# Optimization experiments

Measured on AMD Instinct MI355X. Metric: run time of the kernel, lower is better.

Reference implementation:

```python
import jax, jax.numpy as jnp
import numpy as np

N_NODES = 50000


def _gcn_conv(x, W, b, src, dst, n):
    # PyG GCNConv: linear, then D^{-1/2}(A+I)D^{-1/2} aggregation, then bias.
    x = x @ W  # [N, out]
    loops = jnp.arange(n, dtype=src.dtype)
    src_f = jnp.concatenate([src, loops])  # add self-loops
    dst_f = jnp.concatenate([dst, loops])
    deg = jax.ops.segment_sum(jnp.ones_like(dst_f, dtype=x.dtype), dst_f, num_segments=n)
    dinv = jnp.where(deg > 0, jax.lax.rsqrt(deg), 0.0)
    norm = dinv[src_f] * dinv[dst_f]            # [E+N]
    msg = x[src_f] * norm[:, None]              # gather + scale
    out = jax.ops.segment_sum(msg, dst_f, num_segments=n)  # scatter-add
    return out + b


def setup_inputs() -> dict:
    key = jax.random.key(0)
    k1, k2, k3, k4 = jax.random.split(key, 4)
    ninp = 128
    emb = jax.random.normal(k1, (N_NODES, ninp), dtype=jnp.float32)
    emb = emb.at[0].set(0.0)  # padding_idx=0
    W1 = jax.random.normal(k2, (ninp, 2 * ninp), dtype=jnp.float32) * (1.0 / np.sqrt(ninp))
    b1 = jnp.zeros((2 * ninp,), dtype=jnp.float32)
    W2 = jax.random.normal(k3, (2 * ninp, ninp), dtype=jnp.float32) * (1.0 / np.sqrt(2 * ninp))
    b2 = jnp.zeros((ninp,), dtype=jnp.float32)
    edge_index = jax.random.randint(k4, (2, 800000), 0, N_NODES, dtype=jnp.int64)
    return {"emb": emb, "W1": W1, "b1": b1, "W2": W2, "b2": b2, "edge_index": edge_index}


def reference(emb, W1, b1, W2, b2, edge_index) -> jnp.ndarray:
    src, dst = edge_index[0], edge_index[1]
    h = _gcn_conv(emb, W1, b1, src, dst, N_NODES)   # [N, 2*ninp]
    # dropout in eval mode -> identity
    out = _gcn_conv(h, W2, b2, src, dst, N_NODES)   # [N, ninp]
    return out
```

## Files before the change

### kernel.cpp

```cpp
#include <hip/hip_runtime.h>

#define N_NODES 50000
#define N_EDGES 800000
#define NB 196

typedef unsigned int uint;
typedef short bf16x8 __attribute__((ext_vector_type(8)));
typedef float f32x4 __attribute__((ext_vector_type(4)));

__device__ __forceinline__ ushort f2bf(float f) {
    union { float f; uint u; } v; v.f = f;
    uint r = (v.u + 0x7FFFu + ((v.u >> 16) & 1u)) >> 16;
    return (ushort)r;
}
__device__ __forceinline__ float bf_lo(uint u) { return __uint_as_float(u << 16); }
__device__ __forceinline__ float bf_hi(uint u) { return __uint_as_float(u & 0xFFFF0000u); }

__global__ void k_tobf16(const float* __restrict__ in, uint* __restrict__ out) {
    int t = blockIdx.x * 256 + threadIdx.x;
    const float4* i4 = (const float4*)in + (size_t)t * 2;
    float4 v0 = i4[0], v1 = i4[1];
    uint4 o;
    o.x = (uint)f2bf(v0.x) | ((uint)f2bf(v0.y) << 16);
    o.y = (uint)f2bf(v0.z) | ((uint)f2bf(v0.w) << 16);
    o.z = (uint)f2bf(v1.x) | ((uint)f2bf(v1.y) << 16);
    o.w = (uint)f2bf(v1.z) | ((uint)f2bf(v1.w) << 16);
    ((uint4*)out)[t] = o;
}

__global__ void k_w12(const float* __restrict__ W1, const float* __restrict__ W2,
                      const float* __restrict__ b1, ushort* __restrict__ W12t,
                      float* __restrict__ bvec) {
    int n = threadIdx.x;
    int k = blockIdx.x;
    float s = 0.f;
    if (k < 128) {
        for (int m = 0; m < 256; ++m) s = fmaf(W1[(size_t)k * 256 + m], W2[(size_t)m * 128 + n], s);
        W12t[(size_t)n * 128 + k] = f2bf(s);
    } else {
        for (int m = 0; m < 256; ++m) s = fmaf(b1[m], W2[(size_t)m * 128 + n], s);
        bvec[n] = s;
    }
}


__global__ void k_zero(int* counts) {
    int i = blockIdx.x * 256 + threadIdx.x;
    if (i < N_NODES) counts[i] = 0;
}

__global__ void k_histrank(const int* __restrict__ dst, int* __restrict__ counts,
                           ushort* __restrict__ rank) {
    int e = blockIdx.x * 256 + threadIdx.x;
    if (e < N_EDGES) rank[e] = (ushort)atomicAdd(&counts[dst[e]], 1);
}

__global__ void k_blocksum(const int* __restrict__ counts, int* __restrict__ bsum) {
    __shared__ int lds[256];
    int t = threadIdx.x;
    int i = blockIdx.x * 256 + t;
    int v = (i < N_NODES) ? counts[i] : 0;
    lds[t] = v;
    __syncthreads();
    for (int off = 128; off > 0; off >>= 1) {
        if (t < off) lds[t] += lds[t + off];
        __syncthreads();
    }
    if (t == 0) bsum[blockIdx.x] = lds[0];
}

__global__ void k_scanb(const int* __restrict__ bsum, int* __restrict__ boff) {
    __shared__ int lds[256];
    int t = threadIdx.x;
    int v = (t < NB) ? bsum[t] : 0;
    lds[t] = v;
    __syncthreads();
    for (int off = 1; off < 256; off <<= 1) {
        int o = (t >= off) ? lds[t - off] : 0;
        __syncthreads();
        lds[t] += o;
        __syncthreads();
    }
    if (t < NB) boff[t] = lds[t] - v;
}

__global__ void k_scatter_rp(const int* __restrict__ counts, const int* __restrict__ boff,
                             int* __restrict__ row_ptr, float* __restrict__ dinv) {
    __shared__ int lds[256];
    int t = threadIdx.x;
    int i = blockIdx.x * 256 + t;
    int v = (i < N_NODES) ? counts[i] : 0;
    lds[t] = v;
    __syncthreads();
    for (int off = 1; off < 256; off <<= 1) {
        int o = (t >= off) ? lds[t - off] : 0;
        __syncthreads();
        lds[t] += o;
        __syncthreads();
    }
    if (i < N_NODES) {
        row_ptr[i] = boff[blockIdx.x] + lds[t] - v;
        dinv[i] = rsqrtf((float)(v + 1));
    }
    if (i == 0) row_ptr[N_NODES] = N_EDGES;
}

__global__ void k_fillr(const int* __restrict__ src, const int* __restrict__ dst,
                        const ushort* __restrict__ rank, const int* __restrict__ row_ptr,
                        const float* __restrict__ dinv, uint* __restrict__ csr) {
    int e = blockIdx.x * 256 + threadIdx.x;
    if (e >= N_EDGES) return;
    int s = src[e];
    int pos = row_ptr[dst[e]] + (int)rank[e];
    csr[pos] = ((uint)s << 16) | (uint)f2bf(dinv[s]);
}

template<bool NVEC>
__global__ void k_gather128h(const uint* __restrict__ xh, const uint* __restrict__ csr,
                             const int* __restrict__ rp, const float* __restrict__ dinv,
                             uint* __restrict__ outp, float* __restrict__ nvec) {
    int node = blockIdx.x * 4 + (threadIdx.x >> 6);
    int lane = threadIdx.x & 63;
    int q = lane >> 4;
    int fl = lane & 15;
    int beg = rp[node], end = rp[node + 1];
    const uint4* xb = (const uint4*)xh;
    float a[8];
    #pragma unroll
    for (int i = 0; i < 8; ++i) a[i] = 0.f;
    float sc = 0.f;

    for (int j = beg + q; j < end; j += 16) {
        int j1 = j + 4, j2 = j + 8, j3 = j + 12;
        uint e0 = csr[j];
        uint e1 = (j1 < end) ? csr[j1] : (e0 & 0xFFFF0000u);
        uint e2 = (j2 < end) ? csr[j2] : (e0 & 0xFFFF0000u);
        uint e3 = (j3 < end) ? csr[j3] : (e0 & 0xFFFF0000u);
        int s0 = e0 >> 16, s1 = e1 >> 16, s2 = e2 >> 16, s3 = e3 >> 16;
        float c0 = bf_lo(e0), c1 = bf_lo(e1), c2 = bf_lo(e2), c3 = bf_lo(e3);
        uint4 u0 = xb[(size_t)s0 * 16 + fl];
        uint4 u1 = xb[(size_t)s1 * 16 + fl];
        uint4 u2 = xb[(size_t)s2 * 16 + fl];
        uint4 u3 = xb[(size_t)s3 * 16 + fl];
        sc += c0 + c1 + c2 + c3;
        a[0] = fmaf(c0, bf_lo(u0.x), a[0]); a[1] = fmaf(c0, bf_hi(u0.x), a[1]);
        a[2] = fmaf(c0, bf_lo(u0.y), a[2]); a[3] = fmaf(c0, bf_hi(u0.y), a[3]);
        a[4] = fmaf(c0, bf_lo(u0.z), a[4]); a[5] = fmaf(c0, bf_hi(u0.z), a[5]);
        a[6] = fmaf(c0, bf_lo(u0.w), a[6]); a[7] = fmaf(c0, bf_hi(u0.w), a[7]);
        a[0] = fmaf(c1, bf_lo(u1.x), a[0]); a[1] = fmaf(c1, bf_hi(u1.x), a[1]);
        a[2] = fmaf(c1, bf_lo(u1.y), a[2]); a[3] = fmaf(c1, bf_hi(u1.y), a[3]);
        a[4] = fmaf(c1, bf_lo(u1.z), a[4]); a[5] = fmaf(c1, bf_hi(u1.z), a[5]);
        a[6] = fmaf(c1, bf_lo(u1.w), a[6]); a[7] = fmaf(c1, bf_hi(u1.w), a[7]);
        a[0] = fmaf(c2, bf_lo(u2.x), a[0]); a[1] = fmaf(c2, bf_hi(u2.x), a[1]);
        a[2] = fmaf(c2, bf_lo(u2.y), a[2]); a[3] = fmaf(c2, bf_hi(u2.y), a[3]);
        a[4] = fmaf(c2, bf_lo(u2.z), a[4]); a[5] = fmaf(c2, bf_hi(u2.z), a[5]);
        a[6] = fmaf(c2, bf_lo(u2.w), a[6]); a[7] = fmaf(c2, bf_hi(u2.w), a[7]);
        a[0] = fmaf(c3, bf_lo(u3.x), a[0]); a[1] = fmaf(c3, bf_hi(u3.x), a[1]);
        a[2] = fmaf(c3, bf_lo(u3.y), a[2]); a[3] = fmaf(c3, bf_hi(u3.y), a[3]);
        a[4] = fmaf(c3, bf_lo(u3.z), a[4]); a[5] = fmaf(c3, bf_hi(u3.z), a[5]);
        a[6] = fmaf(c3, bf_lo(u3.w), a[6]); a[7] = fmaf(c3, bf_hi(u3.w), a[7]);
    }
    #pragma unroll
    for (int off = 16; off < 64; off <<= 1) {
        #pragma unroll
        for (int i = 0; i < 8; ++i) a[i] += __shfl_xor(a[i], off);
        if (NVEC) sc += __shfl_xor(sc, off);
    }
    if (q == 0) {
        float dd = dinv[node];
        float dd2 = dd * dd;
        uint4 u = xb[(size_t)node * 16 + fl];
        float s[8] = { bf_lo(u.x), bf_hi(u.x), bf_lo(u.y), bf_hi(u.y),
                       bf_lo(u.z), bf_hi(u.z), bf_lo(u.w), bf_hi(u.w) };
        uint4 p;
        float o0 = fmaf(dd, a[0], dd2 * s[0]), o1 = fmaf(dd, a[1], dd2 * s[1]);
        float o2 = fmaf(dd, a[2], dd2 * s[2]), o3 = fmaf(dd, a[3], dd2 * s[3]);
        float o4 = fmaf(dd, a[4], dd2 * s[4]), o5 = fmaf(dd, a[5], dd2 * s[5]);
        float o6 = fmaf(dd, a[6], dd2 * s[6]), o7 = fmaf(dd, a[7], dd2 * s[7]);
        p.x = (uint)f2bf(o0) | ((uint)f2bf(o1) << 16);
        p.y = (uint)f2bf(o2) | ((uint)f2bf(o3) << 16);
        p.z = (uint)f2bf(o4) | ((uint)f2bf(o5) << 16);
        p.w = (uint)f2bf(o6) | ((uint)f2bf(o7) << 16);
        ((uint4*)outp)[(size_t)node * 16 + fl] = p;
        if (NVEC && fl == 0) nvec[node] = fmaf(dd, sc, dd2);
    }
}

__global__ void __launch_bounds__(256)
k_gemm_out(const ushort* __restrict__ A, const ushort* __restrict__ Wt,
           const float* __restrict__ nvec, const float* __restrict__ bvec,
           const float* __restrict__ b2, float* __restrict__ out) {
    constexpr int K = 128, NC = 128, KC = 4, TPW = 2;
    const int lane = threadIdx.x & 63;
    const int wave = threadIdx.x >> 6;
    const int row0 = blockIdx.x * 16;
    const int r = row0 + (lane & 15);
    const int ksub = (lane >> 4) * 8;

    f32x4 acc[TPW];
    int col[TPW];
    #pragma unroll
    for (int t = 0; t < TPW; ++t) {
        acc[t] = (f32x4){0.f, 0.f, 0.f, 0.f};
        col[t] = (wave * TPW + t) * 16 + (lane & 15);
    }
    #pragma unroll
    for (int kc = 0; kc < KC; ++kc) {
        bf16x8 af = *(const bf16x8*)(A + (size_t)r * K + kc * 32 + ksub);
        #pragma unroll
        for (int t = 0; t < TPW; ++t) {
            bf16x8 bf = *(const bf16x8*)(Wt + (size_t)col[t] * K + kc * 32 + ksub);
            acc[t] = __builtin_amdgcn_mfma_f32_16x16x32_bf16(af, bf, acc[t], 0, 0, 0);
        }
    }
    const int rb = row0 + (lane >> 4) * 4;
    float nv[4];
    #pragma unroll
    for (int e = 0; e < 4; ++e) nv[e] = nvec[rb + e];
    #pragma unroll
    for (int t = 0; t < TPW; ++t) {
        float bv = bvec[col[t]];
        float bb = b2[col[t]];
        #pragma unroll
        for (int e = 0; e < 4; ++e) {
            out[(size_t)(rb + e) * NC + col[t]] = acc[t][e] + nv[e] * bv + bb;
        }
    }
}

extern "C" void kernel_launch(void* const* d_in, const int* in_sizes, int n_in,
                              void* d_out, int out_size, void* d_ws, size_t ws_size,
                              hipStream_t stream) {
    const float* emb = (const float*)d_in[0];
    const float* W1  = (const float*)d_in[1];
    const float* b1  = (const float*)d_in[2];
    const float* W2  = (const float*)d_in[3];
    const float* b2  = (const float*)d_in[4];
    const int*   ei  = (const int*)d_in[5];
    const int* src = ei;
    const int* dst = ei + N_EDGES;

    char* ws = (char*)d_ws;
    float*  dinv    = (float*) (ws);
    int*    counts  = (int*)   (ws + (256ull << 10));
    int*    row_ptr = (int*)   (ws + (512ull << 10));
    int*    bsum    = (int*)   (ws + (768ull << 10));
    int*    boff    = (int*)   (ws + (772ull << 10));
    ushort* rank    = (ushort*)(ws + (1ull << 20));
    uint*   csr     = (uint*)  (ws + (3ull << 20));
    ushort* W12t    = (ushort*)(ws + (6656ull << 10));
    float*  bvec    = (float*) (ws + (6720ull << 10));
    float*  nvec    = (float*) (ws + (6784ull << 10));
    uint*   emb_h   = (uint*)  (ws + (7ull  << 20));
    uint*   G       = (uint*)  (ws + (20ull << 20));
    uint*   G2      = (uint*)  (ws + (33ull << 20));
    float*  out     = (float*)d_out;

    k_tobf16<<<N_NODES * 128 / 8 / 256, 256, 0, stream>>>(emb, emb_h);
    k_w12<<<129, 128, 0, stream>>>(W1, W2, b1, W12t, bvec);

    k_zero<<<NB, 256, 0, stream>>>(counts);
    k_histrank<<<(N_EDGES + 255) / 256, 256, 0, stream>>>(dst, counts, rank);
    k_blocksum<<<NB, 256, 0, stream>>>(counts, bsum);
    k_scanb<<<1, 256, 0, stream>>>(bsum, boff);
    k_scatter_rp<<<NB, 256, 0, stream>>>(counts, boff, row_ptr, dinv);
    k_fillr<<<(N_EDGES + 255) / 256, 256, 0, stream>>>(src, dst, rank, row_ptr, dinv, csr);

    k_gather128h<false><<<12500, 256, 0, stream>>>(emb_h, csr, row_ptr, dinv, G, nullptr);
    k_gather128h<true><<<12500, 256, 0, stream>>>(G, csr, row_ptr, dinv, G2, nvec);
    k_gemm_out<<<N_NODES / 16, 256, 0, stream>>>((const ushort*)G2, W12t, nvec, bvec, b2, out);
}
```

Before: 159.6 us.

## Fuse second gather with output GEMM and merge prep kernels

```diff
diff --git a/kernel.cpp b/kernel.cpp
--- a/kernel.cpp
+++ b/kernel.cpp
@@ -7,6 +7,7 @@
 typedef unsigned int uint;
 typedef short bf16x8 __attribute__((ext_vector_type(8)));
 typedef float f32x4 __attribute__((ext_vector_type(4)));
+typedef uint uint4v __attribute__((ext_vector_type(4)));
 
 __device__ __forceinline__ ushort f2bf(float f) {
     union { float f; uint u; } v; v.f = f;
@@ -16,38 +17,39 @@
 __device__ __forceinline__ float bf_lo(uint u) { return __uint_as_float(u << 16); }
 __device__ __forceinline__ float bf_hi(uint u) { return __uint_as_float(u & 0xFFFF0000u); }
 
-__global__ void k_tobf16(const float* __restrict__ in, uint* __restrict__ out) {
-    int t = blockIdx.x * 256 + threadIdx.x;
-    const float4* i4 = (const float4*)in + (size_t)t * 2;
-    float4 v0 = i4[0], v1 = i4[1];
-    uint4 o;
-    o.x = (uint)f2bf(v0.x) | ((uint)f2bf(v0.y) << 16);
-    o.y = (uint)f2bf(v0.z) | ((uint)f2bf(v0.w) << 16);
-    o.z = (uint)f2bf(v1.x) | ((uint)f2bf(v1.y) << 16);
-    o.w = (uint)f2bf(v1.z) | ((uint)f2bf(v1.w) << 16);
-    ((uint4*)out)[t] = o;
-}
-
-__global__ void k_w12(const float* __restrict__ W1, const float* __restrict__ W2,
-                      const float* __restrict__ b1, ushort* __restrict__ W12t,
-                      float* __restrict__ bvec) {
-    int n = threadIdx.x;
-    int k = blockIdx.x;
-    float s = 0.f;
-    if (k < 128) {
-        for (int m = 0; m < 256; ++m) s = fmaf(W1[(size_t)k * 256 + m], W2[(size_t)m * 128 + n], s);
-        W12t[(size_t)n * 128 + k] = f2bf(s);
+__global__ void k_prep(const float* __restrict__ emb, const float* __restrict__ W1,
+                       const float* __restrict__ W2, const float* __restrict__ b1,
+                       uint* __restrict__ emb_h, ushort* __restrict__ W12t,
+                       float* __restrict__ bvec, int* __restrict__ counts) {
+    int b = blockIdx.x;
+    int tid = threadIdx.x;
+    if (b < 3125) {
+        int t = b * 256 + tid;
+        const float4* i4 = (const float4*)emb + (size_t)t * 2;
+        float4 v0 = i4[0], v1 = i4[1];
+        uint4 o;
+        o.x = (uint)f2bf(v0.x) | ((uint)f2bf(v0.y) << 16);
+        o.y = (uint)f2bf(v0.z) | ((uint)f2bf(v0.w) << 16);
+        o.z = (uint)f2bf(v1.x) | ((uint)f2bf(v1.y) << 16);
+        o.w = (uint)f2bf(v1.z) | ((uint)f2bf(v1.w) << 16);
+        ((uint4*)emb_h)[t] = o;
+    } else if (b < 3125 + NB) {
+        int i = (b - 3125) * 256 + tid;
+        if (i < N_NODES) counts[i] = 0;
     } else {
-        for (int m = 0; m < 256; ++m) s = fmaf(b1[m], W2[(size_t)m * 128 + n], s);
-        bvec[n] = s;
-    }
-}
-
-
-__global__ void k_zero(int* counts) {
-    int i = blockIdx.x * 256 + threadIdx.x;
-    if (i < N_NODES) counts[i] = 0;
-}
+        int k = (b - (3125 + NB)) * 2 + (tid >> 7);
+        int n = tid & 127;
+        float s = 0.f;
+        if (k < 128) {
+            for (int m = 0; m < 256; ++m) s = fmaf(W1[(size_t)k * 256 + m], W2[(size_t)m * 128 + n], s);
+            W12t[(size_t)n * 128 + k] = f2bf(s);
+        } else if (k == 128) {
+            for (int m = 0; m < 256; ++m) s = fmaf(b1[m], W2[(size_t)m * 128 + n], s);
+            bvec[n] = s;
+        }
+    }
+}
+
 
 __global__ void k_histrank(const int* __restrict__ dst, int* __restrict__ counts,
                            ushort* __restrict__ rank) {
@@ -115,115 +117,119 @@
     csr[pos] = ((uint)s << 16) | (uint)f2bf(dinv[s]);
 }
 
-template<bool NVEC>
-__global__ void k_gather128h(const uint* __restrict__ xh, const uint* __restrict__ csr,
-                             const int* __restrict__ rp, const float* __restrict__ dinv,
-                             uint* __restrict__ outp, float* __restrict__ nvec) {
-    int node = blockIdx.x * 4 + (threadIdx.x >> 6);
-    int lane = threadIdx.x & 63;
-    int q = lane >> 4;
-    int fl = lane & 15;
-    int beg = rp[node], end = rp[node + 1];
+__device__ __forceinline__ void gather_core(const uint* __restrict__ xh,
+                                            const uint* __restrict__ csr,
+                                            int beg, int end, int node, float dd,
+                                            int q, int fl, float o[8], float& scn) {
     const uint4* xb = (const uint4*)xh;
     float a[8];
     #pragma unroll
     for (int i = 0; i < 8; ++i) a[i] = 0.f;
     float sc = 0.f;
 
-    for (int j = beg + q; j < end; j += 16) {
-        int j1 = j + 4, j2 = j + 8, j3 = j + 12;
+    for (int j = beg + q; j < end; j += 32) {
         uint e0 = csr[j];
-        uint e1 = (j1 < end) ? csr[j1] : (e0 & 0xFFFF0000u);
-        uint e2 = (j2 < end) ? csr[j2] : (e0 & 0xFFFF0000u);
-        uint e3 = (j3 < end) ? csr[j3] : (e0 & 0xFFFF0000u);
-        int s0 = e0 >> 16, s1 = e1 >> 16, s2 = e2 >> 16, s3 = e3 >> 16;
-        float c0 = bf_lo(e0), c1 = bf_lo(e1), c2 = bf_lo(e2), c3 = bf_lo(e3);
-        uint4 u0 = xb[(size_t)s0 * 16 + fl];
-        uint4 u1 = xb[(size_t)s1 * 16 + fl];
-        uint4 u2 = xb[(size_t)s2 * 16 + fl];
-        uint4 u3 = xb[(size_t)s3 * 16 + fl];
-        sc += c0 + c1 + c2 + c3;
-        a[0] = fmaf(c0, bf_lo(u0.x), a[0]); a[1] = fmaf(c0, bf_hi(u0.x), a[1]);
-        a[2] = fmaf(c0, bf_lo(u0.y), a[2]); a[3] = fmaf(c0, bf_hi(u0.y), a[3]);
-        a[4] = fmaf(c0, bf_lo(u0.z), a[4]); a[5] = fmaf(c0, bf_hi(u0.z), a[5]);
-        a[6] = fmaf(c0, bf_lo(u0.w), a[6]); a[7] = fmaf(c0, bf_hi(u0.w), a[7]);
-        a[0] = fmaf(c1, bf_lo(u1.x), a[0]); a[1] = fmaf(c1, bf_hi(u1.x), a[1]);
-        a[2] = fmaf(c1, bf_lo(u1.y), a[2]); a[3] = fmaf(c1, bf_hi(u1.y), a[3]);
-        a[4] = fmaf(c1, bf_lo(u1.z), a[4]); a[5] = fmaf(c1, bf_hi(u1.z), a[5]);
-        a[6] = fmaf(c1, bf_lo(u1.w), a[6]); a[7] = fmaf(c1, bf_hi(u1.w), a[7]);
-        a[0] = fmaf(c2, bf_lo(u2.x), a[0]); a[1] = fmaf(c2, bf_hi(u2.x), a[1]);
-        a[2] = fmaf(c2, bf_lo(u2.y), a[2]); a[3] = fmaf(c2, bf_hi(u2.y), a[3]);
-        a[4] = fmaf(c2, bf_lo(u2.z), a[4]); a[5] = fmaf(c2, bf_hi(u2.z), a[5]);
-        a[6] = fmaf(c2, bf_lo(u2.w), a[6]); a[7] = fmaf(c2, bf_hi(u2.w), a[7]);
-        a[0] = fmaf(c3, bf_lo(u3.x), a[0]); a[1] = fmaf(c3, bf_hi(u3.x), a[1]);
-        a[2] = fmaf(c3, bf_lo(u3.y), a[2]); a[3] = fmaf(c3, bf_hi(u3.y), a[3]);
-        a[4] = fmaf(c3, bf_lo(u3.z), a[4]); a[5] = fmaf(c3, bf_hi(u3.z), a[5]);
-        a[6] = fmaf(c3, bf_lo(u3.w), a[6]); a[7] = fmaf(c3, bf_hi(u3.w), a[7]);
+        uint def = e0 & 0xFFFF0000u;
+        uint e[8];
+        e[0] = e0;
+        #pragma unroll
+        for (int i = 1; i < 8; ++i) {
+            int ji = j + 4 * i;
+            e[i] = (ji < end) ? csr[ji] : def;
+        }
+        uint4 u[8];
+        #pragma unroll
+        for (int i = 0; i < 8; ++i) u[i] = xb[(size_t)(e[i] >> 16) * 16 + fl];
+        #pragma unroll
+        for (int i = 0; i < 8; ++i) {
+            float c = bf_lo(e[i]);
+            sc += c;
+            a[0] = fmaf(c, bf_lo(u[i].x), a[0]); a[1] = fmaf(c, bf_hi(u[i].x), a[1]);
+            a[2] = fmaf(c, bf_lo(u[i].y), a[2]); a[3] = fmaf(c, bf_hi(u[i].y), a[3]);
+            a[4] = fmaf(c, bf_lo(u[i].z), a[4]); a[5] = fmaf(c, bf_hi(u[i].z), a[5]);
+            a[6] = fmaf(c, bf_lo(u[i].w), a[6]); a[7] = fmaf(c, bf_hi(u[i].w), a[7]);
+        }
     }
     #pragma unroll
     for (int off = 16; off < 64; off <<= 1) {
         #pragma unroll
         for (int i = 0; i < 8; ++i) a[i] += __shfl_xor(a[i], off);
-        if (NVEC) sc += __shfl_xor(sc, off);
-    }
+        sc += __shfl_xor(sc, off);
+    }
+    float dd2 = dd * dd;
+    const uint4* xs = (const uint4*)xh + (size_t)node * 16 + fl;
+    uint4 u = *xs;
+    float s[8] = { bf_lo(u.x), bf_hi(u.x), bf_lo(u.y), bf_hi(u.y),
+                   bf_lo(u.z), bf_hi(u.z), bf_lo(u.w), bf_hi(u.w) };
+    #pragma unroll
+    for (int i = 0; i < 8; ++i) o[i] = fmaf(dd, a[i], dd2 * s[i]);
+    scn = fmaf(dd, sc, dd2);
+}
+
+__global__ void k_gather1(const uint* __restrict__ xh, const uint* __restrict__ csr,
+                          const int* __restrict__ rp, const float* __restrict__ dinv,
+                          uint* __restrict__ outp) {
+    int node = blockIdx.x * 4 + (threadIdx.x >> 6);
+    int lane = threadIdx.x & 63;
+    int q = lane >> 4, fl = lane & 15;
+    int beg = rp[node], end = rp[node + 1];
+    float o[8], scn;
+    gather_core(xh, csr, beg, end, node, dinv[node], q, fl, o, scn);
     if (q == 0) {
-        float dd = dinv[node];
-        float dd2 = dd * dd;
-        uint4 u = xb[(size_t)node * 16 + fl];
-        float s[8] = { bf_lo(u.x), bf_hi(u.x), bf_lo(u.y), bf_hi(u.y),
-                       bf_lo(u.z), bf_hi(u.z), bf_lo(u.w), bf_hi(u.w) };
+        uint4v p;
+        p.x = (uint)f2bf(o[0]) | ((uint)f2bf(o[1]) << 16);
+        p.y = (uint)f2bf(o[2]) | ((uint)f2bf(o[3]) << 16);
+        p.z = (uint)f2bf(o[4]) | ((uint)f2bf(o[5]) << 16);
+        p.w = (uint)f2bf(o[6]) | ((uint)f2bf(o[7]) << 16);
+        __builtin_nontemporal_store(p, (uint4v*)outp + (size_t)node * 16 + fl);
+    }
+}
+
+__global__ void __launch_bounds__(1024)
+k_gather_gemm(const uint* __restrict__ xh, const uint* __restrict__ csr,
+              const int* __restrict__ rp, const float* __restrict__ dinv,
+              const ushort* __restrict__ Wt, const float* __restrict__ bvec,
+              const float* __restrict__ b2, float* __restrict__ out) {
+    __shared__ ushort rows[16 * 128];
+    __shared__ float nvl[16];
+    const int w = threadIdx.x >> 6;
+    const int lane = threadIdx.x & 63;
+    const int node = blockIdx.x * 16 + w;
+    const int q = lane >> 4, fl = lane & 15;
+    const int beg = rp[node], end = rp[node + 1];
+
+    float o[8], scn;
+    gather_core(xh, csr, beg, end, node, dinv[node], q, fl, o, scn);
+    if (q == 0) {
         uint4 p;
-        float o0 = fmaf(dd, a[0], dd2 * s[0]), o1 = fmaf(dd, a[1], dd2 * s[1]);
-        float o2 = fmaf(dd, a[2], dd2 * s[2]), o3 = fmaf(dd, a[3], dd2 * s[3]);
-        float o4 = fmaf(dd, a[4], dd2 * s[4]), o5 = fmaf(dd, a[5], dd2 * s[5]);
-        float o6 = fmaf(dd, a[6], dd2 * s[6]), o7 = fmaf(dd, a[7], dd2 * s[7]);
-        p.x = (uint)f2bf(o0) | ((uint)f2bf(o1) << 16);
-        p.y = (uint)f2bf(o2) | ((uint)f2bf(o3) << 16);
-        p.z = (uint)f2bf(o4) | ((uint)f2bf(o5) << 16);
-        p.w = (uint)f2bf(o6) | ((uint)f2bf(o7) << 16);
-        ((uint4*)outp)[(size_t)node * 16 + fl] = p;
-        if (NVEC && fl == 0) nvec[node] = fmaf(dd, sc, dd2);
-    }
-}
-
-__global__ void __launch_bounds__(256)
-k_gemm_out(const ushort* __restrict__ A, const ushort* __restrict__ Wt,
-           const float* __restrict__ nvec, const float* __restrict__ bvec,
-           const float* __restrict__ b2, float* __restrict__ out) {
-    constexpr int K = 128, NC = 128, KC = 4, TPW = 2;
-    const int lane = threadIdx.x & 63;
-    const int wave = threadIdx.x >> 6;
-    const int row0 = blockIdx.x * 16;
-    const int r = row0 + (lane & 15);
-    const int ksub = (lane >> 4) * 8;
-
-    f32x4 acc[TPW];
-    int col[TPW];
-    #pragma unroll
-    for (int t = 0; t < TPW; ++t) {
-        acc[t] = (f32x4){0.f, 0.f, 0.f, 0.f};
-        col[t] = (wave * TPW + t) * 16 + (lane & 15);
-    }
-    #pragma unroll
-    for (int kc = 0; kc < KC; ++kc) {
-        bf16x8 af = *(const bf16x8*)(A + (size_t)r * K + kc * 32 + ksub);
-        #pragma unroll
-        for (int t = 0; t < TPW; ++t) {
-            bf16x8 bf = *(const bf16x8*)(Wt + (size_t)col[t] * K + kc * 32 + ksub);
-            acc[t] = __builtin_amdgcn_mfma_f32_16x16x32_bf16(af, bf, acc[t], 0, 0, 0);
-        }
-    }
-    const int rb = row0 + (lane >> 4) * 4;
-    float nv[4];
-    #pragma unroll
-    for (int e = 0; e < 4; ++e) nv[e] = nvec[rb + e];
-    #pragma unroll
-    for (int t = 0; t < TPW; ++t) {
-        float bv = bvec[col[t]];
-        float bb = b2[col[t]];
+        p.x = (uint)f2bf(o[0]) | ((uint)f2bf(o[1]) << 16);
+        p.y = (uint)f2bf(o[2]) | ((uint)f2bf(o[3]) << 16);
+        p.z = (uint)f2bf(o[4]) | ((uint)f2bf(o[5]) << 16);
+        p.w = (uint)f2bf(o[6]) | ((uint)f2bf(o[7]) << 16);
+        int idx = (w * 128 + fl * 8) ^ ((w & 7) << 3);
+        *(uint4*)&rows[idx] = p;
+        if (fl == 0) nvl[w] = scn;
+    }
+    __syncthreads();
+
+    if (w < 8) {
+        const int col = w * 16 + (lane & 15);
+        const int ksub = (lane >> 4) * 8;
+        const int row = lane & 15;
+        f32x4 acc = (f32x4){0.f, 0.f, 0.f, 0.f};
+        #pragma unroll
+        for (int kc = 0; kc < 4; ++kc) {
+            int idxr = (row * 128 + kc * 32 + ksub) ^ ((row & 7) << 3);
+            bf16x8 af = *(const bf16x8*)&rows[idxr];
+            bf16x8 bf = *(const bf16x8*)(Wt + (size_t)col * 128 + kc * 32 + ksub);
+            acc = __builtin_amdgcn_mfma_f32_16x16x32_bf16(af, bf, acc, 0, 0, 0);
+        }
+        const int rb = (lane >> 4) * 4;
+        float bv = bvec[col], bb = b2[col];
         #pragma unroll
         for (int e = 0; e < 4; ++e) {
-            out[(size_t)(rb + e) * NC + col[t]] = acc[t][e] + nv[e] * bv + bb;
+            float nv = nvl[rb + e];
+            out[(size_t)(blockIdx.x * 16 + rb + e) * 128 + col] = acc[e] + nv * bv + bb;
         }
     }
 }
@@ -250,23 +256,19 @@
     uint*   csr     = (uint*)  (ws + (3ull << 20));
     ushort* W12t    = (ushort*)(ws + (6656ull << 10));
     float*  bvec    = (float*) (ws + (6720ull << 10));
-    float*  nvec    = (float*) (ws + (6784ull << 10));
     uint*   emb_h   = (uint*)  (ws + (7ull  << 20));
     uint*   G       = (uint*)  (ws + (20ull << 20));
-    uint*   G2      = (uint*)  (ws + (33ull << 20));
     float*  out     = (float*)d_out;
 
-    k_tobf16<<<N_NODES * 128 / 8 / 256, 256, 0, stream>>>(emb, emb_h);
-    k_w12<<<129, 128, 0, stream>>>(W1, W2, b1, W12t, bvec);
-
-    k_zero<<<NB, 256, 0, stream>>>(counts);
+    k_prep<<<3386, 256, 0, stream>>>(emb, W1, W2, b1, emb_h, W12t, bvec, counts);
+
     k_histrank<<<(N_EDGES + 255) / 256, 256, 0, stream>>>(dst, counts, rank);
     k_blocksum<<<NB, 256, 0, stream>>>(counts, bsum);
     k_scanb<<<1, 256, 0, stream>>>(bsum, boff);
     k_scatter_rp<<<NB, 256, 0, stream>>>(counts, boff, row_ptr, dinv);
     k_fillr<<<(N_EDGES + 255) / 256, 256, 0, stream>>>(src, dst, rank, row_ptr, dinv, csr);
 
-    k_gather128h<false><<<12500, 256, 0, stream>>>(emb_h, csr, row_ptr, dinv, G, nullptr);
-    k_gather128h<true><<<12500, 256, 0, stream>>>(G, csr, row_ptr, dinv, G2, nvec);
-    k_gemm_out<<<N_NODES / 16, 256, 0, stream>>>((const ushort*)G2, W12t, nvec, bvec, b2, out);
-}
+    k_gather1<<<12500, 256, 0, stream>>>(emb_h, csr, row_ptr, dinv, G);
+    k_gather_gemm<<<3125, 1024, 0, stream>>>(G, csr, row_ptr, dinv,
+                                             (const ushort*)W12t, bvec, b2, out);
+}
```

After: 171.5 us. 7.5% more time.
